# Kernel optimization log

Hardware: AMD Instinct MI355X
Metric: run time of the kernel (lower is better)

Reference implementation:

```python
import jax, jax.numpy as jnp
import numpy as np

N_NODES = 50000
N_EDGES = 800000
N_GRAPHS = 64
NEG_SLOPE = 0.2
LN_EPS = 1e-5


def setup_inputs() -> dict:
    key = jax.random.key(0)
    ks = jax.random.split(key, 20)
    s = 0.1
    inp = {
        "x": jax.random.normal(ks[0], (N_NODES, 8), jnp.float32),
        "edge_index": jax.random.randint(ks[1], (2, N_EDGES), 0, N_NODES, dtype=jnp.int32),
        "edge_attr": jax.random.uniform(ks[2], (N_EDGES, 1), jnp.float32),
        "batch": jnp.sort(jax.random.randint(ks[3], (N_NODES,), 0, N_GRAPHS, dtype=jnp.int32)),
        "Wl1": jax.random.normal(ks[4], (8, 256), jnp.float32) * s,
        "Wr1": jax.random.normal(ks[5], (8, 256), jnp.float32) * s,
        "We1": jax.random.normal(ks[6], (1, 256), jnp.float32) * s,
        "att1": jax.random.normal(ks[7], (4, 64), jnp.float32) * s,
        "b1": jnp.zeros((256,), jnp.float32),
        "g1": jnp.ones((256,), jnp.float32),
        "beta1": jnp.zeros((256,), jnp.float32),
        "Wl2": jax.random.normal(ks[8], (256, 128), jnp.float32) * s,
        "Wr2": jax.random.normal(ks[9], (256, 128), jnp.float32) * s,
        "We2": jax.random.normal(ks[10], (1, 128), jnp.float32) * s,
        "att2": jax.random.normal(ks[11], (1, 128), jnp.float32) * s,
        "b2": jnp.zeros((128,), jnp.float32),
        "g2": jnp.ones((128,), jnp.float32),
        "beta2": jnp.zeros((128,), jnp.float32),
    }
    return inp


def _gatv2(x, src, dst, ea, Wl, Wr, We, att, bias, heads, ch, concat):
    """PyG GATv2Conv with add_self_loops=True (fill_value='mean' for edge_attr)."""
    n = x.shape[0]
    # self-loop edge_attr = scatter-mean of edge_attr onto target node
    deg = jax.ops.segment_sum(jnp.ones((src.shape[0],), x.dtype), dst, num_segments=n)
    loop_attr = jax.ops.segment_sum(ea, dst, num_segments=n) / jnp.maximum(deg, 1.0)[:, None]
    loop_idx = jnp.arange(n, dtype=src.dtype)
    src2 = jnp.concatenate([src, loop_idx])
    dst2 = jnp.concatenate([dst, loop_idx])
    ea2 = jnp.concatenate([ea, loop_attr], axis=0)           # (E2, edge_dim)

    xl = (x @ Wl).reshape(n, heads, ch)   # source transform
    xr = (x @ Wr).reshape(n, heads, ch)   # target transform
    e = (ea2 @ We).reshape(-1, heads, ch)

    m = xl[src2] + xr[dst2] + e           # (E2, H, C)
    m = jnp.where(m > 0, m, NEG_SLOPE * m)  # LeakyReLU(0.2)
    alpha = jnp.einsum('ehc,hc->eh', m, att)  # (E2, H)
    # softmax over edges grouped by destination node
    amax = jax.ops.segment_max(alpha, dst2, num_segments=n)
    alpha = jnp.exp(alpha - amax[dst2])
    denom = jax.ops.segment_sum(alpha, dst2, num_segments=n)
    alpha = alpha / (denom[dst2] + 1e-16)

    out = jax.ops.segment_sum(alpha[:, :, None] * xl[src2], dst2, num_segments=n)  # (N,H,C)
    out = out.reshape(n, heads * ch) if concat else out.mean(axis=1)
    return out + bias


def _layernorm(x, g, b):
    mu = x.mean(-1, keepdims=True)
    var = ((x - mu) ** 2).mean(-1, keepdims=True)
    return (x - mu) * jax.lax.rsqrt(var + LN_EPS) * g + b


def reference(x, edge_index, edge_attr, batch,
              Wl1, Wr1, We1, att1, b1, g1, beta1,
              Wl2, Wr2, We2, att2, b2, g2, beta2):
    src, dst = edge_index[0], edge_index[1]
    h = _gatv2(x, src, dst, edge_attr, Wl1, Wr1, We1, att1, b1, 4, 64, True)
    h = jax.nn.elu(_layernorm(h, g1, beta1))
    h = _gatv2(h, src, dst, edge_attr, Wl2, Wr2, We2, att2, b2, 1, 128, False)
    h = jax.nn.elu(_layernorm(h, g2, beta2))
    cnt = jax.ops.segment_sum(jnp.ones((h.shape[0],), h.dtype), batch, num_segments=N_GRAPHS)
    pooled = jax.ops.segment_sum(h, batch, num_segments=N_GRAPHS) / jnp.maximum(cnt, 1.0)[:, None]
    return pooled  # (B, 128)
```

## Files before the change

### kernel.cpp

```cpp
#include <hip/hip_runtime.h>
#include <math.h>

#define N_NODES 50000
#define N_EDGES 800000
#define N_GRAPHS 64
#define NREP 32
#define LN_EPS 1e-5f
#define SCAN_BLKS 196

typedef __attribute__((ext_vector_type(8))) short bf16x8;
typedef __attribute__((ext_vector_type(4))) float f32x4;
typedef __attribute__((ext_vector_type(2))) _Float16 half2v;

template <int CTRL>
__device__ __forceinline__ float dppadd(float v) {
  int t = __builtin_amdgcn_update_dpp(0, __float_as_int(v), CTRL, 0xF, 0xF, true);
  return v + __int_as_float(t);
}
__device__ __forceinline__ float red16d(float p) {
  p = dppadd<0xB1>(p);
  p = dppadd<0x4E>(p);
  p = dppadd<0x141>(p);
  p = dppadd<0x140>(p);
  return p;
}
__device__ __forceinline__ float red64(float p) {
  p = red16d(p);
  p += __shfl_xor(p, 16); p += __shfl_xor(p, 32);
  return p;
}

__device__ __forceinline__ unsigned f2bf(float f) {
  unsigned u = __float_as_uint(f);
  return (u + 0x7fffu + ((u >> 16) & 1u)) >> 16;
}
__device__ __forceinline__ float bflo(unsigned u) { return __uint_as_float(u << 16); }
__device__ __forceinline__ float bfhi(unsigned u) { return __uint_as_float(u & 0xffff0000u); }

__device__ __forceinline__ half2v u2h(unsigned u) {
  return __builtin_bit_cast(half2v, u);
}
__device__ __forceinline__ float dot8h(uint4 xh, unsigned w0, unsigned w1,
                                       unsigned w2, unsigned w3) {
#if __has_builtin(__builtin_amdgcn_fdot2)
  float s = __builtin_amdgcn_fdot2(u2h(xh.x), u2h(w0), 0.f, false);
  s = __builtin_amdgcn_fdot2(u2h(xh.y), u2h(w1), s, false);
  s = __builtin_amdgcn_fdot2(u2h(xh.z), u2h(w2), s, false);
  s = __builtin_amdgcn_fdot2(u2h(xh.w), u2h(w3), s, false);
  return s;
#else
  float s = 0.f;
  half2v a;
  a = u2h(xh.x); { half2v b = u2h(w0); s += (float)a.x*(float)b.x + (float)a.y*(float)b.y; }
  a = u2h(xh.y); { half2v b = u2h(w1); s += (float)a.x*(float)b.x + (float)a.y*(float)b.y; }
  a = u2h(xh.z); { half2v b = u2h(w2); s += (float)a.x*(float)b.x + (float)a.y*(float)b.y; }
  a = u2h(xh.w); { half2v b = u2h(w3); s += (float)a.x*(float)b.x + (float)a.y*(float)b.y; }
  return s;
#endif
}

__global__ void k_hist(const int* __restrict__ dst, const float* __restrict__ ea,
                       int* __restrict__ deg, float* __restrict__ easum,
                       int* __restrict__ erank) {
  int e = blockIdx.x * 256 + threadIdx.x;
  if (e >= N_EDGES) return;
  int d = dst[e];
  erank[e] = atomicAdd(&deg[d], 1);
  atomicAdd(&easum[d], ea[e]);
}

__global__ void k_scanA(const int* __restrict__ deg, int* __restrict__ part) {
  int t = threadIdx.x;
  int i = blockIdx.x * 256 + t;
  int len = (i < N_NODES) ? ((deg[i] + 4) & ~3) : 0;
  __shared__ int sm[256];
  sm[t] = len; __syncthreads();
  for (int o = 128; o > 0; o >>= 1) {
    if (t < o) sm[t] += sm[t + o];
    __syncthreads();
  }
  if (t == 0) part[blockIdx.x] = sm[0];
}
__global__ void k_scanB(const int* __restrict__ part, int* __restrict__ base) {
  int t = threadIdx.x;
  __shared__ int sm[256];
  int v = (t < SCAN_BLKS) ? part[t] : 0;
  sm[t] = v; __syncthreads();
  for (int o = 1; o < 256; o <<= 1) {
    int u = (t >= o) ? sm[t - o] : 0;
    __syncthreads();
    sm[t] += u;
    __syncthreads();
  }
  base[t] = (t == 0) ? 0 : sm[t - 1];
}
__global__ void k_scanC(const int* __restrict__ deg, const int* __restrict__ base,
                        const float* __restrict__ easum,
                        int* __restrict__ off2, uint2* __restrict__ sent) {
  int t = threadIdx.x;
  int i = blockIdx.x * 256 + t;
  int d = (i < N_NODES) ? deg[i] : 0;
  int len = (i < N_NODES) ? ((d + 4) & ~3) : 0;
  __shared__ int sm[256];
  sm[t] = len; __syncthreads();
  for (int o = 1; o < 256; o <<= 1) {
    int u = (t >= o) ? sm[t - o] : 0;
    __syncthreads();
    sm[t] += u;
    __syncthreads();
  }
  int incl = sm[t];
  if (i < N_NODES) {
    int b = base[blockIdx.x] + incl - len;
    off2[i] = b;
    float lea = easum[i] / fmaxf((float)d, 1.0f);
    sent[b + d] = make_uint2((unsigned)i, __float_as_uint(lea));
    for (int j = d + 1; j < len; ++j) sent[b + j] = make_uint2(0xFFFFFFFFu, 0u);
  }
  if (i == N_NODES - 1) off2[N_NODES] = base[blockIdx.x] + incl;
}

__global__ void k_scatter(const int* __restrict__ src, const int* __restrict__ dst,
                          const float* __restrict__ ea, const int* __restrict__ off2,
                          const int* __restrict__ erank, uint2* __restrict__ sent) {
  int e = blockIdx.x * 256 + threadIdx.x;
  if (e >= N_EDGES) return;
  int d = dst[e];
  int pos = off2[d] + erank[e];
  sent[pos] = make_uint2((unsigned)src[e], __float_as_uint(ea[e]));
}

__global__ void k_prep(const float* __restrict__ x, uint4* __restrict__ xh,
                       const float* __restrict__ Wl1, unsigned* __restrict__ Wlh,
                       const float* __restrict__ Wl2, const float* __restrict__ Wr2,
                       unsigned short* __restrict__ Btp) {
  int b = blockIdx.x, t = threadIdx.x;
  if (b < SCAN_BLKS) {
    int n = b * 256 + t;
    if (n >= N_NODES) return;
    float4 a = *(const float4*)(x + n * 8);
    float4 c = *(const float4*)(x + n * 8 + 4);
    half2v p0 = {(_Float16)a.x, (_Float16)a.y};
    half2v p1 = {(_Float16)a.z, (_Float16)a.w};
    half2v p2 = {(_Float16)c.x, (_Float16)c.y};
    half2v p3 = {(_Float16)c.z, (_Float16)c.w};
    xh[n] = make_uint4(__builtin_bit_cast(unsigned, p0), __builtin_bit_cast(unsigned, p1),
                       __builtin_bit_cast(unsigned, p2), __builtin_bit_cast(unsigned, p3));
  } else if (b < SCAN_BLKS + 4) {
    int kp = b - SCAN_BLKS;
    half2v h = {(_Float16)Wl1[(2 * kp) * 256 + t], (_Float16)Wl1[(2 * kp + 1) * 256 + t]};
    Wlh[kp * 256 + t] = __builtin_bit_cast(unsigned, h);
  } else {
    int nIdx = b - SCAN_BLKS - 4;
    float v = (nIdx < 128) ? Wl2[t * 128 + nIdx] : Wr2[t * 128 + (nIdx - 128)];
    Btp[nIdx * 256 + t] = (unsigned short)f2bf(v);
  }
}

__global__ __launch_bounds__(256) void k_gat1(
    const float* __restrict__ x, const uint4* __restrict__ xh16,
    const unsigned* __restrict__ Wlh,
    const float* __restrict__ Wr, const float* __restrict__ We,
    const float* __restrict__ att,
    const float* __restrict__ b1, const float* __restrict__ g1,
    const float* __restrict__ be1,
    const int* __restrict__ off2, const uint2* __restrict__ sent,
    unsigned* __restrict__ h1b) {
  int lane = threadIdx.x & 63;
  int wv = __builtin_amdgcn_readfirstlane(threadIdx.x >> 6);
  int n = blockIdx.x * 4 + wv;
  int c0 = lane * 4;

  float4 wev = *(const float4*)(We + c0);
  float4 atv = *(const float4*)(att + c0);

  float xn[8];
  {
    float4 a = *(const float4*)(x + n * 8);
    float4 b = *(const float4*)(x + n * 8 + 4);
    xn[0]=a.x; xn[1]=a.y; xn[2]=a.z; xn[3]=a.w;
    xn[4]=b.x; xn[5]=b.y; xn[6]=b.z; xn[7]=b.w;
  }
  float xr0=0.f, xr1=0.f, xr2=0.f, xr3=0.f;
#pragma unroll
  for (int k = 0; k < 8; ++k) {
    float4 wr = *(const float4*)(Wr + k * 256 + c0);
    xr0 += xn[k]*wr.x; xr1 += xn[k]*wr.y; xr2 += xn[k]*wr.z; xr3 += xn[k]*wr.w;
  }
  uint4 wk0 = *(const uint4*)(Wlh + 0 * 256 + c0);
  uint4 wk1 = *(const uint4*)(Wlh + 1 * 256 + c0);
  uint4 wk2 = *(const uint4*)(Wlh + 2 * 256 + c0);
  uint4 wk3 = *(const uint4*)(Wlh + 3 * 256 + c0);

  int beg   = __builtin_amdgcn_readfirstlane(off2[n]);
  int pairs = __builtin_amdgcn_readfirstlane((off2[n + 1] - beg) >> 1);

  float den = 0.f, ac0=0.f, ac1=0.f, ac2=0.f, ac3=0.f;

  uint4 pr = *(const uint4*)(sent + beg);
  int   sA = __builtin_amdgcn_readfirstlane((int)pr.x);
  int   sB = __builtin_amdgcn_readfirstlane((int)pr.z);
  float eA = __uint_as_float(pr.y), eB = __uint_as_float(pr.w);
  uint4 xA = xh16[max(sA, 0)];
  uint4 xB = xh16[max(sB, 0)];

  for (int p = 0; p < pairs; ++p) {
    int   csA = sA, csB = sB;
    float ceA = eA, ceB = eB;
    uint4 cxA = xA, cxB = xB;
    if (p + 1 < pairs) {
      pr = *(const uint4*)(sent + beg + 2 * (p + 1));
      sA = __builtin_amdgcn_readfirstlane((int)pr.x);
      sB = __builtin_amdgcn_readfirstlane((int)pr.z);
      eA = __uint_as_float(pr.y); eB = __uint_as_float(pr.w);
      xA = xh16[max(sA, 0)];
      xB = xh16[max(sB, 0)];
    }
    float vA0 = dot8h(cxA, wk0.x, wk1.x, wk2.x, wk3.x);
    float vA1 = dot8h(cxA, wk0.y, wk1.y, wk2.y, wk3.y);
    float vA2 = dot8h(cxA, wk0.z, wk1.z, wk2.z, wk3.z);
    float vA3 = dot8h(cxA, wk0.w, wk1.w, wk2.w, wk3.w);
    float vB0 = dot8h(cxB, wk0.x, wk1.x, wk2.x, wk3.x);
    float vB1 = dot8h(cxB, wk0.y, wk1.y, wk2.y, wk3.y);
    float vB2 = dot8h(cxB, wk0.z, wk1.z, wk2.z, wk3.z);
    float vB3 = dot8h(cxB, wk0.w, wk1.w, wk2.w, wk3.w);

    float mA0 = vA0 + fmaf(ceA, wev.x, xr0); mA0 = fmaxf(mA0, 0.2f*mA0);
    float mA1 = vA1 + fmaf(ceA, wev.y, xr1); mA1 = fmaxf(mA1, 0.2f*mA1);
    float mA2 = vA2 + fmaf(ceA, wev.z, xr2); mA2 = fmaxf(mA2, 0.2f*mA2);
    float mA3 = vA3 + fmaf(ceA, wev.w, xr3); mA3 = fmaxf(mA3, 0.2f*mA3);
    float mB0 = vB0 + fmaf(ceB, wev.x, xr0); mB0 = fmaxf(mB0, 0.2f*mB0);
    float mB1 = vB1 + fmaf(ceB, wev.y, xr1); mB1 = fmaxf(mB1, 0.2f*mB1);
    float mB2 = vB2 + fmaf(ceB, wev.z, xr2); mB2 = fmaxf(mB2, 0.2f*mB2);
    float mB3 = vB3 + fmaf(ceB, wev.w, xr3); mB3 = fmaxf(mB3, 0.2f*mB3);

    float pA = mA0*atv.x + mA1*atv.y + mA2*atv.z + mA3*atv.w;
    float pB = mB0*atv.x + mB1*atv.y + mB2*atv.z + mB3*atv.w;
    pA = red16d(pA);
    pB = red16d(pB);

    float wA = (csA >= 0) ? __expf(pA) : 0.f;
    float wB = (csB >= 0) ? __expf(pB) : 0.f;
    den += wA + wB;
    ac0 = fmaf(wA, vA0, fmaf(wB, vB0, ac0));
    ac1 = fmaf(wA, vA1, fmaf(wB, vB1, ac1));
    ac2 = fmaf(wA, vA2, fmaf(wB, vB2, ac2));
    ac3 = fmaf(wA, vA3, fmaf(wB, vB3, ac3));
  }

  float inv = 1.0f / (den + 1e-16f);
  float4 bv = *(const float4*)(b1 + c0);
  float o0 = ac0*inv + bv.x, o1 = ac1*inv + bv.y;
  float o2 = ac2*inv + bv.z, o3 = ac3*inv + bv.w;
  float mu = red64(o0 + o1 + o2 + o3) * (1.0f / 256.0f);
  float d0 = o0-mu, d1 = o1-mu, d2 = o2-mu, d3 = o3-mu;
  float rstd = rsqrtf(red64(d0*d0 + d1*d1 + d2*d2 + d3*d3) * (1.0f/256.0f) + LN_EPS);
  float4 gv  = *(const float4*)(g1 + c0);
  float4 bev = *(const float4*)(be1 + c0);
  float y0 = d0*rstd*gv.x + bev.x; y0 = y0 > 0.f ? y0 : __expf(y0) - 1.0f;
  float y1 = d1*rstd*gv.y + bev.y; y1 = y1 > 0.f ? y1 : __expf(y1) - 1.0f;
  float y2 = d2*rstd*gv.z + bev.z; y2 = y2 > 0.f ? y2 : __expf(y2) - 1.0f;
  float y3 = d3*rstd*gv.w + bev.w; y3 = y3 > 0.f ? y3 : __expf(y3) - 1.0f;
  unsigned lo = f2bf(y0) | (f2bf(y1) << 16);
  unsigned hi = f2bf(y2) | (f2bf(y3) << 16);
  *(uint2*)(h1b + (size_t)n * 128 + lane * 2) = make_uint2(lo, hi);
}

__global__ __launch_bounds__(256) void k_gemm2(
    const unsigned* __restrict__ h1b, const unsigned short* __restrict__ Btp,
    unsigned short* __restrict__ xl2b, float* __restrict__ xr2) {
  __shared__ unsigned short Ash[64][264];
  __shared__ unsigned short Bsh[64][264];
  int t = threadIdx.x;
  int bm0 = blockIdx.x * 64;
  int lane = t & 63, w = t >> 6;
  int lm = lane & 15, lk = (lane >> 4) * 8;

#pragma unroll
  for (int i = 0; i < 8; ++i) {
    int idx = t + 256 * i;
    int row = idx >> 5, c4 = idx & 31;
    int gm = bm0 + row;
    uint4 va = (gm < N_NODES) ? *(const uint4*)(h1b + (size_t)gm * 128 + c4 * 4)
                              : make_uint4(0,0,0,0);
    *(uint4*)(&Ash[row][c4 * 8]) = va;
  }

  for (int pnl = 0; pnl < 4; ++pnl) {
    int n0 = pnl * 64;
#pragma unroll
    for (int i = 0; i < 8; ++i) {
      int idx = t + 256 * i;
      int row = idx >> 5, c4 = idx & 31;
      uint4 vb = *(const uint4*)((const unsigned*)Btp + (size_t)(n0 + row) * 128 + c4 * 4);
      *(uint4*)(&Bsh[row][c4 * 8]) = vb;
    }
    __syncthreads();

    f32x4 acc[4];
#pragma unroll
    for (int i = 0; i < 4; ++i) acc[i] = (f32x4){0.f,0.f,0.f,0.f};
#pragma unroll
    for (int kk = 0; kk < 8; ++kk) {
      bf16x8 a = *(const bf16x8*)(&Ash[16*w + lm][kk*32 + lk]);
#pragma unroll
      for (int tt = 0; tt < 4; ++tt) {
        bf16x8 b = *(const bf16x8*)(&Bsh[16*tt + lm][kk*32 + lk]);
        acc[tt] = __builtin_amdgcn_mfma_f32_16x16x32_bf16(a, b, acc[tt], 0, 0, 0);
      }
    }

#pragma unroll
    for (int tt = 0; tt < 4; ++tt) {
#pragma unroll
      for (int r = 0; r < 4; ++r) {
        int node = bm0 + 16*w + (lane >> 4) * 4 + r;
        if (node < N_NODES) {
          int colg = n0 + tt * 16 + lm;
          float v = acc[tt][r];
          if (colg < 128) xl2b[(size_t)node * 128 + colg] = (unsigned short)f2bf(v);
          else            xr2 [(size_t)node * 128 + (colg - 128)] = v;
        }
      }
    }
    __syncthreads();
  }
}

__global__ __launch_bounds__(256) void k_gat2(
    const unsigned* __restrict__ xl2b, const float* __restrict__ xr2,
    const float* __restrict__ We, const float* __restrict__ att,
    const float* __restrict__ b2, const float* __restrict__ g2,
    const float* __restrict__ be2,
    const int* __restrict__ off2, const uint2* __restrict__ sent,
    const int* __restrict__ batch,
    float* __restrict__ pool, float* __restrict__ cnt) {
  int tid = threadIdx.x;
  int lane = tid & 63;
  int wv = __builtin_amdgcn_readfirstlane(tid >> 6);
  int row = lane >> 4, col = lane & 15;
  int n = blockIdx.x * 4 + wv;
  int c0 = col * 8;
  int cu0 = col * 4;

  float wev[8], at[8], xr[8];
  *(float4*)(wev)     = *(const float4*)(We + c0);
  *(float4*)(wev + 4) = *(const float4*)(We + c0 + 4);
  *(float4*)(at)      = *(const float4*)(att + c0);
  *(float4*)(at + 4)  = *(const float4*)(att + c0 + 4);
  *(float4*)(xr)      = *(const float4*)(xr2 + (size_t)n * 128 + c0);
  *(float4*)(xr + 4)  = *(const float4*)(xr2 + (size_t)n * 128 + c0 + 4);

  int beg   = __builtin_amdgcn_readfirstlane(off2[n]);
  int quads = __builtin_amdgcn_readfirstlane((off2[n + 1] - beg) >> 2);

  float den = 0.f;
  float ac[8] = {0,0,0,0,0,0,0,0};

  int s0=-1,s1=-1,s2=-1,s3=-1,s4=-1,s5=-1;
  float e0=0,e1=0,e2=0,e3=0,e4=0,e5=0;
  uint4 z = make_uint4(0,0,0,0);
  uint4 u0=z,u1=z,u2=z,u3=z,u4=z,u5=z;
#define LOADSTAGE(S,E,U,Q) { uint2 tt_ = sent[beg + (Q) * 4 + row]; \
    S = (int)tt_.x; E = __uint_as_float(tt_.y); \
    U = *(const uint4*)(xl2b + (size_t)max(S, 0) * 64 + cu0); }
  { LOADSTAGE(s0,e0,u0,0) }
  if (quads > 1) { LOADSTAGE(s1,e1,u1,1) }
  if (quads > 2) { LOADSTAGE(s2,e2,u2,2) }
  if (quads > 3) { LOADSTAGE(s3,e3,u3,3) }
  if (quads > 4) { LOADSTAGE(s4,e4,u4,4) }
  if (quads > 5) { LOADSTAGE(s5,e5,u5,5) }

  for (int q = 0; q < quads; ++q) {
    int cs = s0; float ce = e0; uint4 cu = u0;
    s0=s1; e0=e1; u0=u1;
    s1=s2; e1=e2; u1=u2;
    s2=s3; e2=e3; u2=u3;
    s3=s4; e3=e4; u3=u4;
    s4=s5; e4=e5; u4=u5;
    if (q + 6 < quads) { LOADSTAGE(s5,e5,u5,q+6) }
    float v[8];
    v[0]=bflo(cu.x); v[1]=bfhi(cu.x); v[2]=bflo(cu.y); v[3]=bfhi(cu.y);
    v[4]=bflo(cu.z); v[5]=bfhi(cu.z); v[6]=bflo(cu.w); v[7]=bfhi(cu.w);
    float p = 0.f;
#pragma unroll
    for (int j = 0; j < 8; ++j) {
      float m = v[j] + fmaf(ce, wev[j], xr[j]);
      m = fmaxf(m, 0.2f * m);
      p = fmaf(m, at[j], p);
    }
    p = red16d(p);
    float w = (cs >= 0) ? __expf(p) : 0.f;
    den += w;
#pragma unroll
    for (int j = 0; j < 8; ++j) ac[j] = fmaf(w, v[j], ac[j]);
  }
#undef LOADSTAGE
  den += __shfl_xor(den, 16); den += __shfl_xor(den, 32);
#pragma unroll
  for (int j = 0; j < 8; ++j) {
    ac[j] += __shfl_xor(ac[j], 16);
    ac[j] += __shfl_xor(ac[j], 32);
  }

  float inv = 1.0f / (den + 1e-16f);
  float o[8], y[8];
  float bv[8], gv[8], bev[8];
  *(float4*)(bv)      = *(const float4*)(b2 + c0);
  *(float4*)(bv + 4)  = *(const float4*)(b2 + c0 + 4);
  *(float4*)(gv)      = *(const float4*)(g2 + c0);
  *(float4*)(gv + 4)  = *(const float4*)(g2 + c0 + 4);
  *(float4*)(bev)     = *(const float4*)(be2 + c0);
  *(float4*)(bev + 4) = *(const float4*)(be2 + c0 + 4);
  float osum = 0.f;
#pragma unroll
  for (int j = 0; j < 8; ++j) { o[j] = ac[j] * inv + bv[j]; osum += o[j]; }
  float mu = red64(osum) * (1.0f / 512.0f);
  float vsum = 0.f;
#pragma unroll
  for (int j = 0; j < 8; ++j) { o[j] -= mu; vsum += o[j] * o[j]; }
  float rstd = rsqrtf(red64(vsum) * (1.0f / 512.0f) + LN_EPS);
#pragma unroll
  for (int j = 0; j < 8; ++j) {
    float t2 = o[j] * rstd * gv[j] + bev[j];
    y[j] = t2 > 0.f ? t2 : __expf(t2) - 1.0f;
  }

  __shared__ float pbuf[4][128];
  __shared__ int gbuf[4];
  if (row == 0) {
#pragma unroll
    for (int j = 0; j < 8; ++j) pbuf[wv][c0 + j] = y[j];
  }
  if (lane == 0) gbuf[wv] = batch[n];
  __syncthreads();
  if (wv == 0) {
    int r = blockIdx.x & (NREP - 1);
    int ch = lane;
    float acc0 = pbuf[0][ch], acc1 = pbuf[0][ch+64];
    int cg = gbuf[0], cn = 1;
#pragma unroll
    for (int i = 1; i < 4; ++i) {
      if (gbuf[i] == cg) { acc0 += pbuf[i][ch]; acc1 += pbuf[i][ch+64]; cn++; }
      else {
        float* pp = pool + ((size_t)(r * N_GRAPHS + cg)) * 128;
        atomicAdd(pp + ch, acc0); atomicAdd(pp + ch + 64, acc1);
        if (lane == 0) atomicAdd(&cnt[r * N_GRAPHS + cg], (float)cn);
        cg = gbuf[i]; acc0 = pbuf[i][ch]; acc1 = pbuf[i][ch+64]; cn = 1;
      }
    }
    float* pp = pool + ((size_t)(r * N_GRAPHS + cg)) * 128;
    atomicAdd(pp + ch, acc0); atomicAdd(pp + ch + 64, acc1);
    if (lane == 0) atomicAdd(&cnt[r * N_GRAPHS + cg], (float)cn);
  }
}

__global__ void k_final(const float* __restrict__ pool, const float* __restrict__ cnt,
                        float* __restrict__ out) {
  int idx = blockIdx.x * 256 + threadIdx.x;
  if (idx >= N_GRAPHS * 128) return;
  int g = idx >> 7, c = idx & 127;
  float s = 0.f, nn = 0.f;
#pragma unroll
  for (int r = 0; r < NREP; ++r) {
    s  += pool[((size_t)(r * N_GRAPHS + g)) * 128 + c];
    nn += cnt[r * N_GRAPHS + g];
  }
  out[idx] = s / fmaxf(nn, 1.0f);
}

extern "C" void kernel_launch(void* const* d_in, const int* in_sizes, int n_in,
                              void* d_out, int out_size, void* d_ws, size_t ws_size,
                              hipStream_t stream) {
  const float* x    = (const float*)d_in[0];
  const int*   ei   = (const int*)  d_in[1];
  const float* ea   = (const float*)d_in[2];
  const int*   batch= (const int*)  d_in[3];
  const float* Wl1  = (const float*)d_in[4];
  const float* Wr1  = (const float*)d_in[5];
  const float* We1  = (const float*)d_in[6];
  const float* att1 = (const float*)d_in[7];
  const float* b1   = (const float*)d_in[8];
  const float* g1   = (const float*)d_in[9];
  const float* be1  = (const float*)d_in[10];
  const float* Wl2  = (const float*)d_in[11];
  const float* Wr2  = (const float*)d_in[12];
  const float* We2  = (const float*)d_in[13];
  const float* att2 = (const float*)d_in[14];
  const float* b2   = (const float*)d_in[15];
  const float* g2   = (const float*)d_in[16];
  const float* be2  = (const float*)d_in[17];
  const int* srcp = ei;
  const int* dstp = ei + N_EDGES;

  const int MAXE2 = N_EDGES + 4 * N_NODES;

  char* ws = (char*)d_ws;
  size_t off = 0;
  auto alloc = [&](size_t bytes) {
    char* p = ws + off; off += (bytes + 15) & ~(size_t)15; return p;
  };
  int*            deg   = (int*)           alloc((size_t)N_NODES * 4);
  float*          easum = (float*)         alloc((size_t)N_NODES * 4);
  int*            off2  = (int*)           alloc((size_t)(N_NODES + 1) * 4);
  int*            part  = (int*)           alloc((size_t)256 * 4);
  int*            base  = (int*)           alloc((size_t)257 * 4);
  int*            erank = (int*)           alloc((size_t)N_EDGES * 4);
  uint2*          sent  = (uint2*)         alloc((size_t)MAXE2 * 8);
  uint4*          xh16  = (uint4*)         alloc((size_t)N_NODES * 16);
  unsigned*       Wlh   = (unsigned*)      alloc((size_t)4 * 256 * 4);
  unsigned*       h1b   = (unsigned*)      alloc((size_t)N_NODES * 128 * 4);
  unsigned short* xl2b  = (unsigned short*)alloc((size_t)N_NODES * 128 * 2);
  float*          xr2   = (float*)         alloc((size_t)N_NODES * 128 * 4);
  unsigned short* Btp   = (unsigned short*)alloc((size_t)256 * 256 * 2);
  float*          pool  = (float*)         alloc((size_t)NREP * N_GRAPHS * 128 * 4);
  float*          cnt   = (float*)         alloc((size_t)NREP * N_GRAPHS * 4);

  (void)hipMemsetAsync(deg, 0, (char*)off2 - (char*)deg, stream);
  (void)hipMemsetAsync(pool, 0, ((char*)cnt + (((size_t)NREP*N_GRAPHS*4 + 15) & ~(size_t)15))
                           - (char*)pool, stream);

  k_hist    <<<N_EDGES / 256, 256, 0, stream>>>(dstp, ea, deg, easum, erank);
  k_prep    <<<SCAN_BLKS + 4 + 256, 256, 0, stream>>>(x, xh16, Wl1, Wlh, Wl2, Wr2, Btp);
  k_scanA   <<<SCAN_BLKS, 256, 0, stream>>>(deg, part);
  k_scanB   <<<1, 256, 0, stream>>>(part, base);
  k_scanC   <<<SCAN_BLKS, 256, 0, stream>>>(deg, base, easum, off2, sent);
  k_scatter <<<N_EDGES / 256, 256, 0, stream>>>(srcp, dstp, ea, off2, erank, sent);
  k_gat1    <<<N_NODES / 4, 256, 0, stream>>>(x, xh16, Wlh, Wr1, We1, att1, b1, g1, be1,
                                              off2, sent, h1b);
  k_gemm2   <<<(N_NODES + 63) / 64, 256, 0, stream>>>(h1b, Btp, xl2b, xr2);
  k_gat2    <<<N_NODES / 4, 256, 0, stream>>>((const unsigned*)xl2b, xr2, We2, att2,
                                              b2, g2, be2,
                                              off2, sent, batch, pool, cnt);
  k_final   <<<(N_GRAPHS * 128) / 256, 256, 0, stream>>>(pool, cnt, (float*)d_out);
}
```

Measured before the change: 395.5 us.

## Fuse hist with prep, fold scan base into scanC, unroll gat2 edge loop

Merges the edge histogram and the prep conversion into one launch, and drops the single-block scanB by having each scanC block reduce the partial sums of the blocks before it. The attention vectors are pre-scaled by log2(e) so exp2f replaces __expf. The gat2 edge loop now handles two edge quads per iteration, with interleaved DPP reductions, to expose more ILP. Together these cut two kernel launches and shorten the dependency chains, at the cost of redundant prefix reductions in every scanC block and higher register pressure in gat2.

```diff
diff --git a/kernel.cpp b/kernel.cpp
--- a/kernel.cpp
+++ b/kernel.cpp
@@ -7,6 +7,8 @@
 #define NREP 32
 #define LN_EPS 1e-5f
 #define SCAN_BLKS 196
+#define HIST_BLKS 3125
+#define LOG2E 1.44269504088896340736f
 
 typedef __attribute__((ext_vector_type(8))) short bf16x8;
 typedef __attribute__((ext_vector_type(4))) float f32x4;
@@ -23,6 +25,12 @@
   p = dppadd<0x141>(p);
   p = dppadd<0x140>(p);
   return p;
+}
+__device__ __forceinline__ void red16x2d(float& a, float& b) {
+  a = dppadd<0xB1>(a);  b = dppadd<0xB1>(b);
+  a = dppadd<0x4E>(a);  b = dppadd<0x4E>(b);
+  a = dppadd<0x141>(a); b = dppadd<0x141>(b);
+  a = dppadd<0x140>(a); b = dppadd<0x140>(b);
 }
 __device__ __forceinline__ float red64(float p) {
   p = red16d(p);
@@ -59,14 +67,42 @@
 #endif
 }
 
-__global__ void k_hist(const int* __restrict__ dst, const float* __restrict__ ea,
-                       int* __restrict__ deg, float* __restrict__ easum,
-                       int* __restrict__ erank) {
-  int e = blockIdx.x * 256 + threadIdx.x;
-  if (e >= N_EDGES) return;
-  int d = dst[e];
-  erank[e] = atomicAdd(&deg[d], 1);
-  atomicAdd(&easum[d], ea[e]);
+__global__ void k_histprep(const int* __restrict__ dst, const float* __restrict__ ea,
+                           int* __restrict__ deg, float* __restrict__ easum,
+                           int* __restrict__ erank,
+                           const float* __restrict__ x, uint4* __restrict__ xh,
+                           const float* __restrict__ Wl1, unsigned* __restrict__ Wlh,
+                           const float* __restrict__ Wl2, const float* __restrict__ Wr2,
+                           unsigned short* __restrict__ Btp) {
+  int b = blockIdx.x, t = threadIdx.x;
+  if (b < HIST_BLKS) {
+    int e = b * 256 + t;
+    int d = dst[e];
+    erank[e] = atomicAdd(&deg[d], 1);
+    atomicAdd(&easum[d], ea[e]);
+    return;
+  }
+  int pb = b - HIST_BLKS;
+  if (pb < SCAN_BLKS) {
+    int n = pb * 256 + t;
+    if (n >= N_NODES) return;
+    float4 a = *(const float4*)(x + n * 8);
+    float4 c = *(const float4*)(x + n * 8 + 4);
+    half2v p0 = {(_Float16)a.x, (_Float16)a.y};
+    half2v p1 = {(_Float16)a.z, (_Float16)a.w};
+    half2v p2 = {(_Float16)c.x, (_Float16)c.y};
+    half2v p3 = {(_Float16)c.z, (_Float16)c.w};
+    xh[n] = make_uint4(__builtin_bit_cast(unsigned, p0), __builtin_bit_cast(unsigned, p1),
+                       __builtin_bit_cast(unsigned, p2), __builtin_bit_cast(unsigned, p3));
+  } else if (pb < SCAN_BLKS + 4) {
+    int kp = pb - SCAN_BLKS;
+    half2v h = {(_Float16)Wl1[(2 * kp) * 256 + t], (_Float16)Wl1[(2 * kp + 1) * 256 + t]};
+    Wlh[kp * 256 + t] = __builtin_bit_cast(unsigned, h);
+  } else {
+    int nIdx = pb - SCAN_BLKS - 4;
+    float v = (nIdx < 128) ? Wl2[t * 128 + nIdx] : Wr2[t * 128 + (nIdx - 128)];
+    Btp[nIdx * 256 + t] = (unsigned short)f2bf(v);
+  }
 }
 
 __global__ void k_scanA(const int* __restrict__ deg, int* __restrict__ part) {
@@ -81,27 +117,23 @@
   }
   if (t == 0) part[blockIdx.x] = sm[0];
 }
-__global__ void k_scanB(const int* __restrict__ part, int* __restrict__ base) {
-  int t = threadIdx.x;
-  __shared__ int sm[256];
-  int v = (t < SCAN_BLKS) ? part[t] : 0;
-  sm[t] = v; __syncthreads();
-  for (int o = 1; o < 256; o <<= 1) {
-    int u = (t >= o) ? sm[t - o] : 0;
-    __syncthreads();
-    sm[t] += u;
-    __syncthreads();
-  }
-  base[t] = (t == 0) ? 0 : sm[t - 1];
-}
-__global__ void k_scanC(const int* __restrict__ deg, const int* __restrict__ base,
+__global__ void k_scanC(const int* __restrict__ deg, const int* __restrict__ part,
                         const float* __restrict__ easum,
                         int* __restrict__ off2, uint2* __restrict__ sent) {
   int t = threadIdx.x;
+  __shared__ int sm[256];
+  __shared__ int basev;
+  int pv = (t < blockIdx.x) ? part[t] : 0;
+  sm[t] = pv; __syncthreads();
+  for (int o = 128; o > 0; o >>= 1) {
+    if (t < o) sm[t] += sm[t + o];
+    __syncthreads();
+  }
+  if (t == 0) basev = sm[0];
+  __syncthreads();
   int i = blockIdx.x * 256 + t;
   int d = (i < N_NODES) ? deg[i] : 0;
   int len = (i < N_NODES) ? ((d + 4) & ~3) : 0;
-  __shared__ int sm[256];
   sm[t] = len; __syncthreads();
   for (int o = 1; o < 256; o <<= 1) {
     int u = (t >= o) ? sm[t - o] : 0;
@@ -111,13 +143,13 @@
   }
   int incl = sm[t];
   if (i < N_NODES) {
-    int b = base[blockIdx.x] + incl - len;
+    int b = basev + incl - len;
     off2[i] = b;
     float lea = easum[i] / fmaxf((float)d, 1.0f);
     sent[b + d] = make_uint2((unsigned)i, __float_as_uint(lea));
     for (int j = d + 1; j < len; ++j) sent[b + j] = make_uint2(0xFFFFFFFFu, 0u);
   }
-  if (i == N_NODES - 1) off2[N_NODES] = base[blockIdx.x] + incl;
+  if (i == N_NODES - 1) off2[N_NODES] = basev + incl;
 }
 
 __global__ void k_scatter(const int* __restrict__ src, const int* __restrict__ dst,
@@ -128,33 +160,6 @@
   int d = dst[e];
   int pos = off2[d] + erank[e];
   sent[pos] = make_uint2((unsigned)src[e], __float_as_uint(ea[e]));
-}
-
-__global__ void k_prep(const float* __restrict__ x, uint4* __restrict__ xh,
-                       const float* __restrict__ Wl1, unsigned* __restrict__ Wlh,
-                       const float* __restrict__ Wl2, const float* __restrict__ Wr2,
-                       unsigned short* __restrict__ Btp) {
-  int b = blockIdx.x, t = threadIdx.x;
-  if (b < SCAN_BLKS) {
-    int n = b * 256 + t;
-    if (n >= N_NODES) return;
-    float4 a = *(const float4*)(x + n * 8);
-    float4 c = *(const float4*)(x + n * 8 + 4);
-    half2v p0 = {(_Float16)a.x, (_Float16)a.y};
-    half2v p1 = {(_Float16)a.z, (_Float16)a.w};
-    half2v p2 = {(_Float16)c.x, (_Float16)c.y};
-    half2v p3 = {(_Float16)c.z, (_Float16)c.w};
-    xh[n] = make_uint4(__builtin_bit_cast(unsigned, p0), __builtin_bit_cast(unsigned, p1),
-                       __builtin_bit_cast(unsigned, p2), __builtin_bit_cast(unsigned, p3));
-  } else if (b < SCAN_BLKS + 4) {
-    int kp = b - SCAN_BLKS;
-    half2v h = {(_Float16)Wl1[(2 * kp) * 256 + t], (_Float16)Wl1[(2 * kp + 1) * 256 + t]};
-    Wlh[kp * 256 + t] = __builtin_bit_cast(unsigned, h);
-  } else {
-    int nIdx = b - SCAN_BLKS - 4;
-    float v = (nIdx < 128) ? Wl2[t * 128 + nIdx] : Wr2[t * 128 + (nIdx - 128)];
-    Btp[nIdx * 256 + t] = (unsigned short)f2bf(v);
-  }
 }
 
 __global__ __launch_bounds__(256) void k_gat1(
@@ -173,6 +178,7 @@
 
   float4 wev = *(const float4*)(We + c0);
   float4 atv = *(const float4*)(att + c0);
+  atv.x *= LOG2E; atv.y *= LOG2E; atv.z *= LOG2E; atv.w *= LOG2E;
 
   float xn[8];
   {
@@ -236,11 +242,10 @@
 
     float pA = mA0*atv.x + mA1*atv.y + mA2*atv.z + mA3*atv.w;
     float pB = mB0*atv.x + mB1*atv.y + mB2*atv.z + mB3*atv.w;
-    pA = red16d(pA);
-    pB = red16d(pB);
-
-    float wA = (csA >= 0) ? __expf(pA) : 0.f;
-    float wB = (csB >= 0) ? __expf(pB) : 0.f;
+    red16x2d(pA, pB);
+
+    float wA = (csA >= 0) ? exp2f(pA) : 0.f;
+    float wB = (csB >= 0) ? exp2f(pB) : 0.f;
     den += wA + wB;
     ac0 = fmaf(wA, vA0, fmaf(wB, vB0, ac0));
     ac1 = fmaf(wA, vA1, fmaf(wB, vB1, ac1));
@@ -348,6 +353,8 @@
   *(float4*)(wev + 4) = *(const float4*)(We + c0 + 4);
   *(float4*)(at)      = *(const float4*)(att + c0);
   *(float4*)(at + 4)  = *(const float4*)(att + c0 + 4);
+#pragma unroll
+  for (int j = 0; j < 8; ++j) at[j] *= LOG2E;
   *(float4*)(xr)      = *(const float4*)(xr2 + (size_t)n * 128 + c0);
   *(float4*)(xr + 4)  = *(const float4*)(xr2 + (size_t)n * 128 + c0 + 4);
 
@@ -371,29 +378,36 @@
   if (quads > 4) { LOADSTAGE(s4,e4,u4,4) }
   if (quads > 5) { LOADSTAGE(s5,e5,u5,5) }
 
-  for (int q = 0; q < quads; ++q) {
-    int cs = s0; float ce = e0; uint4 cu = u0;
-    s0=s1; e0=e1; u0=u1;
-    s1=s2; e1=e2; u1=u2;
-    s2=s3; e2=e3; u2=u3;
-    s3=s4; e3=e4; u3=u4;
-    s4=s5; e4=e5; u4=u5;
-    if (q + 6 < quads) { LOADSTAGE(s5,e5,u5,q+6) }
-    float v[8];
-    v[0]=bflo(cu.x); v[1]=bfhi(cu.x); v[2]=bflo(cu.y); v[3]=bfhi(cu.y);
-    v[4]=bflo(cu.z); v[5]=bfhi(cu.z); v[6]=bflo(cu.w); v[7]=bfhi(cu.w);
-    float p = 0.f;
+  for (int q = 0; q < quads; q += 2) {
+    int csA = s0; float ceA = e0; uint4 cuA = u0;
+    int csB = s1; float ceB = e1; uint4 cuB = u1;
+    s0=s2; e0=e2; u0=u2;  s1=s3; e1=e3; u1=u3;
+    s2=s4; e2=e4; u2=u4;  s3=s5; e3=e5; u3=u5;
+    if (q + 6 < quads) { LOADSTAGE(s4,e4,u4,q+6) } else { s4 = -1; e4 = 0.f; u4 = z; }
+    if (q + 7 < quads) { LOADSTAGE(s5,e5,u5,q+7) } else { s5 = -1; e5 = 0.f; u5 = z; }
+
+    float vA[8], vB[8];
+    vA[0]=bflo(cuA.x); vA[1]=bfhi(cuA.x); vA[2]=bflo(cuA.y); vA[3]=bfhi(cuA.y);
+    vA[4]=bflo(cuA.z); vA[5]=bfhi(cuA.z); vA[6]=bflo(cuA.w); vA[7]=bfhi(cuA.w);
+    vB[0]=bflo(cuB.x); vB[1]=bfhi(cuB.x); vB[2]=bflo(cuB.y); vB[3]=bfhi(cuB.y);
+    vB[4]=bflo(cuB.z); vB[5]=bfhi(cuB.z); vB[6]=bflo(cuB.w); vB[7]=bfhi(cuB.w);
+    float pA = 0.f, pB = 0.f;
 #pragma unroll
     for (int j = 0; j < 8; ++j) {
-      float m = v[j] + fmaf(ce, wev[j], xr[j]);
-      m = fmaxf(m, 0.2f * m);
-      p = fmaf(m, at[j], p);
+      float mA = vA[j] + fmaf(ceA, wev[j], xr[j]);
+      mA = fmaxf(mA, 0.2f * mA);
+      pA = fmaf(mA, at[j], pA);
+      float mB = vB[j] + fmaf(ceB, wev[j], xr[j]);
+      mB = fmaxf(mB, 0.2f * mB);
+      pB = fmaf(mB, at[j], pB);
     }
-    p = red16d(p);
-    float w = (cs >= 0) ? __expf(p) : 0.f;
-    den += w;
-#pragma unroll
-    for (int j = 0; j < 8; ++j) ac[j] = fmaf(w, v[j], ac[j]);
+    red16x2d(pA, pB);
+    float wA = (csA >= 0) ? exp2f(pA) : 0.f;
+    float wB = (csB >= 0) ? exp2f(pB) : 0.f;
+    den += wA + wB;
+#pragma unroll
+    for (int j = 0; j < 8; ++j)
+      ac[j] = fmaf(wA, vA[j], fmaf(wB, vB[j], ac[j]));
   }
 #undef LOADSTAGE
   den += __shfl_xor(den, 16); den += __shfl_xor(den, 32);
@@ -504,7 +518,6 @@
   float*          easum = (float*)         alloc((size_t)N_NODES * 4);
   int*            off2  = (int*)           alloc((size_t)(N_NODES + 1) * 4);
   int*            part  = (int*)           alloc((size_t)256 * 4);
-  int*            base  = (int*)           alloc((size_t)257 * 4);
   int*            erank = (int*)           alloc((size_t)N_EDGES * 4);
   uint2*          sent  = (uint2*)         alloc((size_t)MAXE2 * 8);
   uint4*          xh16  = (uint4*)         alloc((size_t)N_NODES * 16);
@@ -520,12 +533,11 @@
   (void)hipMemsetAsync(pool, 0, ((char*)cnt + (((size_t)NREP*N_GRAPHS*4 + 15) & ~(size_t)15))
                            - (char*)pool, stream);
 
-  k_hist    <<<N_EDGES / 256, 256, 0, stream>>>(dstp, ea, deg, easum, erank);
-  k_prep    <<<SCAN_BLKS + 4 + 256, 256, 0, stream>>>(x, xh16, Wl1, Wlh, Wl2, Wr2, Btp);
+  k_histprep<<<HIST_BLKS + SCAN_BLKS + 4 + 256, 256, 0, stream>>>(
+      dstp, ea, deg, easum, erank, x, xh16, Wl1, Wlh, Wl2, Wr2, Btp);
   k_scanA   <<<SCAN_BLKS, 256, 0, stream>>>(deg, part);
-  k_scanB   <<<1, 256, 0, stream>>>(part, base);
-  k_scanC   <<<SCAN_BLKS, 256, 0, stream>>>(deg, base, easum, off2, sent);
-  k_scatter <<<N_EDGES / 256, 256, 0, stream>>>(srcp, dstp, ea, off2, erank, sent);
+  k_scanC   <<<SCAN_BLKS, 256, 0, stream>>>(deg, part, easum, off2, sent);
+  k_scatter <<<HIST_BLKS, 256, 0, stream>>>(srcp, dstp, ea, off2, erank, sent);
   k_gat1    <<<N_NODES / 4, 256, 0, stream>>>(x, xh16, Wlh, Wr1, We1, att1, b1, g1, be1,
                                               off2, sent, h1b);
   k_gemm2   <<<(N_NODES + 63) / 64, 256, 0, stream>>>(h1b, Btp, xl2b, xr2);
```

Result: slower. 411.7 us (+4.1%).
